# Kernel optimization log

Hardware: AMD Instinct MI355X
Metric: run time of the kernel (lower is better)

Reference implementation:

```python
import jax, jax.numpy as jnp
import numpy as np
from jax import lax

N_STEPS = 8          # fixed-step discretization of t in [0, 1]
GN_GROUPS = 32       # group_norm(width) -> GroupNorm(min(32, width), width)
GN_EPS = 1e-5

# Tsit5 Butcher tableau (c nodes, a stage coeffs, b solution weights; b7 = 0)
_C = (0.161, 0.327, 0.9, 0.9800255409045097, 1.0)
_A = (
    (0.161,),
    (-0.008480655492356989, 0.335480655492357),
    (2.8971530571054935, -6.359448489975075, 4.3622954328695815),
    (5.325864828439257, -11.748883564062828, 7.4955393428898365, -0.09249506636175525),
    (5.86145544294642, -12.92096931784711, 8.159367898576159, -0.071584973281401, -0.028269050394068383),
)
_B = (0.09646076681806523, 0.01, 0.4798896504144996, 1.379008574103742, -3.290069515436081, 2.324710524099774)


def _conv3x3(x, w, b):
    # x: [B, Cin, H, W], w: [Cout, Cin, 3, 3], padding=1, stride=1
    y = lax.conv_general_dilated(x, w, (1, 1), ((1, 1), (1, 1)),
                                 dimension_numbers=("NCHW", "OIHW", "NCHW"))
    return y + b[None, :, None, None]


def _group_norm(x, scale, bias):
    B, C, H, W = x.shape
    xr = x.reshape(B, GN_GROUPS, C // GN_GROUPS, H, W)
    mu = xr.mean(axis=(2, 3, 4), keepdims=True)
    var = xr.var(axis=(2, 3, 4), keepdims=True)
    xn = ((xr - mu) * lax.rsqrt(var + GN_EPS)).reshape(B, C, H, W)
    return xn * scale[None, :, None, None] + bias[None, :, None, None]


def _ode_func(t, x, p):
    # ConcatConv2D: prepend a channel filled with scalar t
    B, _, H, W = x.shape
    tt = jnp.full((B, 1, H, W), t, dtype=x.dtype)
    h = _conv3x3(jnp.concatenate([tt, x], axis=1), p["conv1_w"], p["conv1_b"])
    h = jax.nn.relu(_group_norm(h, p["gn1_scale"], p["gn1_bias"]))
    tt2 = jnp.full((B, 1, H, W), t, dtype=x.dtype)
    h = _conv3x3(jnp.concatenate([tt2, h], axis=1), p["conv2_w"], p["conv2_b"])
    return _group_norm(h, p["gn2_scale"], p["gn2_bias"])


def _tsit5_solve(x, p):
    dt = jnp.float32(1.0 / N_STEPS)

    def step(carry, _):
        y, t = carry
        k1 = _ode_func(t, y, p)
        k2 = _ode_func(t + _C[0] * dt, y + dt * (_A[0][0] * k1), p)
        k3 = _ode_func(t + _C[1] * dt, y + dt * (_A[1][0] * k1 + _A[1][1] * k2), p)
        k4 = _ode_func(t + _C[2] * dt,
                       y + dt * (_A[2][0] * k1 + _A[2][1] * k2 + _A[2][2] * k3), p)
        k5 = _ode_func(t + _C[3] * dt,
                       y + dt * (_A[3][0] * k1 + _A[3][1] * k2 + _A[3][2] * k3 + _A[3][3] * k4), p)
        k6 = _ode_func(t + _C[4] * dt,
                       y + dt * (_A[4][0] * k1 + _A[4][1] * k2 + _A[4][2] * k3
                                 + _A[4][3] * k4 + _A[4][4] * k5), p)
        y_next = y + dt * (_B[0] * k1 + _B[1] * k2 + _B[2] * k3
                           + _B[3] * k4 + _B[4] * k5 + _B[5] * k6)
        return (y_next, t + dt), None

    (yT, _), _ = lax.scan(step, (x, jnp.float32(0.0)), None, length=N_STEPS)
    return yT


def setup_inputs() -> dict:
    key = jax.random.key(0)
    ks = jax.random.split(key, 5)
    B, C, H, W = 64, 64, 32, 32
    cin = C + 1  # concat t channel
    fan_in = cin * 9
    lim = 1.0 / np.sqrt(fan_in)
    x = jax.random.normal(ks[0], (B, C, H, W), dtype=jnp.float32)
    conv1_w = jax.random.uniform(ks[1], (C, cin, 3, 3), jnp.float32, -lim, lim)
    conv1_b = jax.random.uniform(ks[2], (C,), jnp.float32, -lim, lim)
    conv2_w = jax.random.uniform(ks[3], (C, cin, 3, 3), jnp.float32, -lim, lim)
    conv2_b = jax.random.uniform(ks[4], (C,), jnp.float32, -lim, lim)
    return {
        "x": x,
        "conv1_w": conv1_w, "conv1_b": conv1_b,
        "gn1_scale": jnp.ones((C,), jnp.float32), "gn1_bias": jnp.zeros((C,), jnp.float32),
        "conv2_w": conv2_w, "conv2_b": conv2_b,
        "gn2_scale": jnp.ones((C,), jnp.float32), "gn2_bias": jnp.zeros((C,), jnp.float32),
    }


def reference(x, conv1_w, conv1_b, gn1_scale, gn1_bias, conv2_w, conv2_b, gn2_scale, gn2_bias):
    p = {"conv1_w": conv1_w, "conv1_b": conv1_b, "gn1_scale": gn1_scale, "gn1_bias": gn1_bias,
         "conv2_w": conv2_w, "conv2_b": conv2_b, "gn2_scale": gn2_scale, "gn2_bias": gn2_bias}
    return _tsit5_solve(x, p)
```

## Files before the change

kernel.cpp:

```cpp
#include <hip/hip_runtime.h>

typedef __attribute__((ext_vector_type(8))) _Float16 f16x8;
typedef __attribute__((ext_vector_type(4))) float f32x4;
typedef unsigned short u16;

#define BB 64
#define NPIX 1024
#define NELEM (BB*64*NPIX)
#define NRT 8

#define PLANE (6*34*64)

__device__ __forceinline__ int swz8(int c8, int p) {
    return (c8 + ((p + (p >> 2)) & 7)) & 7;
}

__device__ __forceinline__ u16 f2h(float x) {
    _Float16 h = (_Float16)x;
    return __builtin_bit_cast(u16, h);
}
__device__ __forceinline__ float h2f(u16 u) {
    return (float)__builtin_bit_cast(_Float16, u);
}

__global__ __launch_bounds__(256) void prep_w_k(
    const float* __restrict__ w, u16* __restrict__ wt)
{
    int t = blockIdx.x*256 + threadIdx.x;
    if (t >= 4608) return;
    int lane = t & 63;
    int f = t >> 6;
    int g = f & 7;
    int tap = f >> 3;
    int coutblk = g & 3;
    int kc = g >> 2;
    int cout = coutblk*16 + (lane & 15);
    int quad = lane >> 4;
    u16 v[8];
#pragma unroll
    for (int j = 0; j < 8; ++j) {
        int cin = kc*32 + quad*8 + j;
        v[j] = f2h(w[((size_t)cout*65 + (cin+1))*9 + tap]);
    }
    u16* dst = wt + ((size_t)tap*4096 + (g*64 + lane)*8);
    *(ushort4*)(dst)     = make_ushort4(v[0], v[1], v[2], v[3]);
    *(ushort4*)(dst + 4) = make_ushort4(v[4], v[5], v[6], v[7]);
}

__global__ __launch_bounds__(256) void smap_k(
    const float* __restrict__ w, float* __restrict__ smap)
{
    int t = blockIdx.x*256 + threadIdx.x;
    int cout = t >> 10;
    int pix = t & 1023;
    int y = pix >> 5, x = pix & 31;
    float s = 0.f;
#pragma unroll
    for (int dy = 0; dy < 3; ++dy)
#pragma unroll
        for (int dx = 0; dx < 3; ++dx) {
            int yy = y + dy - 1, xx = x + dx - 1;
            if ((unsigned)yy < 32u && (unsigned)xx < 32u)
                s += w[(size_t)cout*65*9 + dy*3 + dx];
        }
    smap[t] = s;
}

template<int MODE, int NK, bool WRITEY>
__global__ __launch_bounds__(512, 4) void conv_mfma_k(
    const float* __restrict__ src0, const u16* __restrict__ srcb,
    const u16* __restrict__ kp0, const u16* __restrict__ kp1,
    const u16* __restrict__ kp2, const u16* __restrict__ kp3,
    const u16* __restrict__ kp4, const u16* __restrict__ kp5,
    float* __restrict__ yout,
    float* __restrict__ part,
    const float* __restrict__ gns, const float* __restrict__ gnb,
    const float* __restrict__ gks, const float* __restrict__ gkb,
    const u16* __restrict__ wt, const float* __restrict__ smap,
    const float* __restrict__ bias, u16* __restrict__ out, float tval,
    int slot_in, int slot_out,
    float a1, float a2, float a3, float a4, float a5, float a6)
{
    __shared__ u16 lds_in[PLANE];
    __shared__ float kaf[6][64];
    __shared__ float kbf[64];
    __shared__ float ps[256], pss[256];
    __shared__ float rg[64], rgq[64];

    const int rt  = blockIdx.x;
    const int b   = blockIdx.y;
    const int tid = threadIdx.x;
    const int wv   = tid >> 6;
    const int lane = tid & 63;
    const int quad = lane >> 4;
    const int n15  = lane & 15;
    const int r0   = wv & 3;
    const int mh   = wv >> 2;

    float4 Y0[2], Y1[2];
    ushort4 H0[2], H1[2];

    auto prim_load = [&](int h) {
#pragma unroll
        for (int uu = 0; uu < 2; ++uu) {
            int ur = tid + uu*512;
            if (ur >= 768) continue;
            int u = h*768 + ur;
            int q4 = u & 7;
            int t2 = u >> 3;
            int rr = t2 % 6;
            int c2 = t2 / 6;
            int gr = rt*4 + rr - 1;
            if ((unsigned)gr < 32u) {
                const size_t base = (((size_t)b*64 + c2*2)*32 + gr)*32 + q4*4;
                if constexpr (MODE == 2) {
                    H0[uu] = *(const ushort4*)(srcb + base);
                    H1[uu] = *(const ushort4*)(srcb + base + 1024);
                } else {
                    Y0[uu] = *(const float4*)(src0 + base);
                    Y1[uu] = *(const float4*)(src0 + base + 1024);
                }
            }
        }
    };

    auto stage_finish = [&](int h) {
#pragma unroll
        for (int uu = 0; uu < 2; ++uu) {
            int ur = tid + uu*512;
            if (ur >= 768) continue;
            int u = h*768 + ur;
            int q4 = u & 7;
            int t2 = u >> 3;
            int rr = t2 % 6;
            int c2 = t2 / 6;
            int gr = rt*4 + rr - 1;
            bool ok = (unsigned)gr < 32u;
            int ch0 = c2*2, ch1 = ch0 + 1;
            float4 a0 = make_float4(0.f,0.f,0.f,0.f), a1v = a0;
            if (ok) {
                const size_t base = (((size_t)b*64 + ch0)*32 + gr)*32 + q4*4;
                if constexpr (MODE == 2) {
                    float A0 = kaf[0][ch0], B0 = kbf[ch0];
                    float A1 = kaf[0][ch1], B1 = kbf[ch1];
                    a0.x = fmaxf(fmaf(h2f(H0[uu].x),A0,B0), 0.f);
                    a0.y = fmaxf(fmaf(h2f(H0[uu].y),A0,B0), 0.f);
                    a0.z = fmaxf(fmaf(h2f(H0[uu].z),A0,B0), 0.f);
                    a0.w = fmaxf(fmaf(h2f(H0[uu].w),A0,B0), 0.f);
                    a1v.x = fmaxf(fmaf(h2f(H1[uu].x),A1,B1), 0.f);
                    a1v.y = fmaxf(fmaf(h2f(H1[uu].y),A1,B1), 0.f);
                    a1v.z = fmaxf(fmaf(h2f(H1[uu].z),A1,B1), 0.f);
                    a1v.w = fmaxf(fmaf(h2f(H1[uu].w),A1,B1), 0.f);
                } else {
                    a0 = Y0[uu]; a1v = Y1[uu];
                    if constexpr (MODE == 1) {
                        float f0 = kbf[ch0], f1 = kbf[ch1];
                        a0.x += f0; a0.y += f0; a0.z += f0; a0.w += f0;
                        a1v.x += f1; a1v.y += f1; a1v.z += f1; a1v.w += f1;
                        const u16* kps[6] = {kp0, kp1, kp2, kp3, kp4, kp5};
#pragma unroll
                        for (int jj = 0; jj < NK; ++jj) {
                            ushort4 kv0 = *(const ushort4*)(kps[jj] + base);
                            ushort4 kv1 = *(const ushort4*)(kps[jj] + base + 1024);
                            float fa0 = kaf[jj][ch0], fa1 = kaf[jj][ch1];
                            a0.x = fmaf(fa0, h2f(kv0.x), a0.x);
                            a0.y = fmaf(fa0, h2f(kv0.y), a0.y);
                            a0.z = fmaf(fa0, h2f(kv0.z), a0.z);
                            a0.w = fmaf(fa0, h2f(kv0.w), a0.w);
                            a1v.x = fmaf(fa1, h2f(kv1.x), a1v.x);
                            a1v.y = fmaf(fa1, h2f(kv1.y), a1v.y);
                            a1v.z = fmaf(fa1, h2f(kv1.z), a1v.z);
                            a1v.w = fmaf(fa1, h2f(kv1.w), a1v.w);
                        }
                    }
                }
                if constexpr (WRITEY) {
                    if (rr >= 1 && rr <= 4) {
                        *(float4*)(yout + base)        = a0;
                        *(float4*)(yout + base + 1024) = a1v;
                    }
                }
            }
            float v0[4] = {a0.x, a0.y, a0.z, a0.w};
            float v1[4] = {a1v.x, a1v.y, a1v.z, a1v.w};
            int c8 = c2 >> 2, cl = c2 & 3;
            int pbase = rr*34 + 1 + q4*4;
#pragma unroll
            for (int j = 0; j < 4; ++j) {
                int p = pbase + j;
                int au = p*64 + swz8(c8, p)*8 + cl*2;
                *(unsigned*)&lds_in[au] =
                    (unsigned)f2h(v0[j]) | ((unsigned)f2h(v1[j]) << 16);
            }
        }
    };

    f32x4 acc[2][2] = {};
    auto mfma_kc = [&](int kc) {
#pragma unroll 3
        for (int tap = 0; tap < 9; ++tap) {
            const int dy = tap / 3;
            const int dx = tap - dy*3;
            const int rowoff = (r0 + dy)*34 + dx;
            const u16* wtap = wt + (size_t)tap*4096;
            f16x8 A[2], Bf[2];
#pragma unroll
            for (int mt = 0; mt < 2; ++mt)
                A[mt] = *(const f16x8*)
                    &wtap[((kc*4 + mh*2 + mt)*64 + lane)*8];
#pragma unroll
            for (int nt = 0; nt < 2; ++nt) {
                int p = rowoff + nt*16 + n15;
                Bf[nt] = *(const f16x8*)&lds_in[p*64 + swz8(kc*4 + quad, p)*8];
            }
#pragma unroll
            for (int mt = 0; mt < 2; ++mt)
#pragma unroll
                for (int nt = 0; nt < 2; ++nt)
                    acc[mt][nt] = __builtin_amdgcn_mfma_f32_16x16x32_f16(
                        A[mt], Bf[nt], acc[mt][nt], 0, 0, 0);
        }
    };

    prim_load(0);

    if constexpr (MODE == 1) {
        if (tid < 64) {
            const float aa[6] = {a1, a2, a3, a4, a5, a6};
            int g = tid >> 1;
            float acb = 0.f;
#pragma unroll
            for (int jj = 0; jj < NK; ++jj) {
                const float4* pp = (const float4*)
                    (part + ((((size_t)(1+jj)*64 + b)*32 + g)*NRT)*2);
                float4 x0 = pp[0], x1 = pp[1], x2 = pp[2], x3 = pp[3];
                float S  = x0.x+x0.z + x1.x+x1.z + x2.x+x2.z + x3.x+x3.z;
                float SS = x0.y+x0.w + x1.y+x1.w + x2.y+x2.w + x3.y+x3.w;
                float mu   = S * (1.f/2048.f);
                float var  = SS * (1.f/2048.f) - mu*mu;
                float rstd = rsqrtf(var + 1e-5f);
                float a = gks[tid]*rstd;
                float c = gkb[tid] - mu*a;
                kaf[jj][tid] = aa[jj]*a;
                acb += aa[jj]*c;
            }
            kbf[tid] = acb;
        }
    } else if constexpr (MODE == 2) {
        if (tid < 64) {
            int g = tid >> 1;
            const float4* pp = (const float4*)
                (part + ((((size_t)slot_in*64 + b)*32 + g)*NRT)*2);
            float4 x0 = pp[0], x1 = pp[1], x2 = pp[2], x3 = pp[3];
            float S  = x0.x+x0.z + x1.x+x1.z + x2.x+x2.z + x3.x+x3.z;
            float SS = x0.y+x0.w + x1.y+x1.w + x2.y+x2.w + x3.y+x3.w;
            float mu   = S * (1.f/2048.f);
            float var  = SS * (1.f/2048.f) - mu*mu;
            float rstd = rsqrtf(var + 1e-5f);
            float a = gns[tid]*rstd;
            kaf[0][tid] = a;
            kbf[tid] = gnb[tid] - mu*a;
        }
    }
    __syncthreads();

    stage_finish(0);
    if (tid < 384) {
        int c2 = tid & 31;
        int t3 = tid >> 5;
        int rr = t3 % 6;
        int e  = t3 / 6;
        int p  = rr*34 + e*33;
        int au = p*64 + swz8(c2 >> 2, p)*8 + (c2 & 3)*2;
        *(unsigned*)&lds_in[au] = 0u;
    }
    __syncthreads();

    prim_load(1);
    mfma_kc(0);
    stage_finish(1);
    __syncthreads();

    mfma_kc(1);

    const int orow = rt*4 + r0;
#pragma unroll
    for (int mt = 0; mt < 2; ++mt) {
#pragma unroll
        for (int r = 0; r < 4; ++r) {
            int cout = mh*32 + mt*16 + quad*4 + r;
            float bs = bias[cout];
            const float* sp = smap + (size_t)cout*1024 + orow*32;
            u16* op = out + (((size_t)b*64 + cout)*32 + orow)*32;
            float v0 = acc[mt][0][r] + bs + tval*sp[n15];
            float v1 = acc[mt][1][r] + bs + tval*sp[16 + n15];
            op[n15]      = f2h(v0);
            op[16 + n15] = f2h(v1);
            float s = v0 + v1;
            float q = v0*v0 + v1*v1;
            s += __shfl_xor(s, 1); q += __shfl_xor(q, 1);
            s += __shfl_xor(s, 2); q += __shfl_xor(q, 2);
            s += __shfl_xor(s, 4); q += __shfl_xor(q, 4);
            s += __shfl_xor(s, 8); q += __shfl_xor(q, 8);
            if (n15 == 0) { ps[r0*64 + cout] = s; pss[r0*64 + cout] = q; }
        }
    }
    __syncthreads();
    if (tid < 64) {
        rg[tid]  = ps[tid]  + ps[64+tid]  + ps[128+tid]  + ps[192+tid];
        rgq[tid] = pss[tid] + pss[64+tid] + pss[128+tid] + pss[192+tid];
    }
    __syncthreads();
    if (tid < 32) {
        float S  = rg[2*tid]  + rg[2*tid+1];
        float SS = rgq[2*tid] + rgq[2*tid+1];
        float* pp = part + ((((size_t)slot_out*64 + b)*32 + tid)*NRT + rt)*2;
        pp[0] = S; pp[1] = SS;
    }
}

__global__ __launch_bounds__(256) void final_combine_k(
    const float* __restrict__ ysrc, float* __restrict__ ydst,
    const u16* __restrict__ k0, const u16* __restrict__ k1,
    const u16* __restrict__ k2, const u16* __restrict__ k3,
    const u16* __restrict__ k4, const u16* __restrict__ k5,
    const float* __restrict__ part,
    const float* __restrict__ g2s, const float* __restrict__ g2b,
    float b0, float b1, float b2, float b3, float b4, float b5)
{
    const int bidx = blockIdx.x;
    const int b = bidx >> 6, ch = bidx & 63, g = ch >> 1;
    const int t = threadIdx.x;
    __shared__ float rs[6][2];
    if (t < 12) {
        int jj = t >> 1, st = t & 1;
        const float* pp = part + ((((size_t)(1+jj)*64 + b)*32 + g)*NRT)*2 + st;
        float v = 0.f;
#pragma unroll
        for (int q = 0; q < NRT; ++q) v += pp[2*q];
        rs[jj][st] = v;
    }
    __syncthreads();
    const float bb[6] = {b0, b1, b2, b3, b4, b5};
    float fa[6], fcs = 0.f;
#pragma unroll
    for (int jj = 0; jj < 6; ++jj) {
        float mu   = rs[jj][0] * (1.f/2048.f);
        float var  = rs[jj][1] * (1.f/2048.f) - mu*mu;
        float rstd = rsqrtf(var + 1e-5f);
        float a = g2s[ch]*rstd;
        float c = g2b[ch] - mu*a;
        fa[jj] = bb[jj]*a;
        fcs   += bb[jj]*c;
    }
    const size_t base = ((size_t)bidx*256 + t)*4;
    float4 r = *(const float4*)(ysrc + base);
    r.x += fcs; r.y += fcs; r.z += fcs; r.w += fcs;
    const u16* kp[6] = {k0, k1, k2, k3, k4, k5};
#pragma unroll
    for (int jj = 0; jj < 6; ++jj) {
        ushort4 kv = *(const ushort4*)(kp[jj] + base);
        r.x = fmaf(fa[jj], h2f(kv.x), r.x);
        r.y = fmaf(fa[jj], h2f(kv.y), r.y);
        r.z = fmaf(fa[jj], h2f(kv.z), r.z);
        r.w = fmaf(fa[jj], h2f(kv.w), r.w);
    }
    *(float4*)(ydst + base) = r;
}


static const double A_[5][5] = {
    {0.161, 0, 0, 0, 0},
    {-0.008480655492356989, 0.335480655492357, 0, 0, 0},
    {2.8971530571054935, -6.359448489975075, 4.3622954328695815, 0, 0},
    {5.325864828439257, -11.748883564062828, 7.4955393428898365, -0.09249506636175525, 0},
    {5.86145544294642, -12.92096931784711, 8.159367898576159, -0.071584973281401, -0.028269050394068383},
};
static const double B_[6] = {
    0.09646076681806523, 0.01, 0.4798896504144996,
    1.379008574103742, -3.290069515436081, 2.324710524099774,
};
static const double C_[5] = {0.161, 0.327, 0.9, 0.9800255409045097, 1.0};

extern "C" void kernel_launch(void* const* d_in, const int* in_sizes, int n_in,
                              void* d_out, int out_size, void* d_ws, size_t ws_size,
                              hipStream_t stream)
{
    const float* x   = (const float*)d_in[0];
    const float* c1w = (const float*)d_in[1];
    const float* c1b = (const float*)d_in[2];
    const float* g1s = (const float*)d_in[3];
    const float* g1b = (const float*)d_in[4];
    const float* c2w = (const float*)d_in[5];
    const float* c2b = (const float*)d_in[6];
    const float* g2s = (const float*)d_in[7];
    const float* g2b = (const float*)d_in[8];

    float* y  = (float*)d_out;
    u16*   wsb = (u16*)d_ws;
    u16*   h  = wsb;
    u16*   k[6];
    for (int i = 0; i < 6; ++i) k[i] = wsb + (size_t)(1 + i) * NELEM;
    u16*   wt1   = wsb + (size_t)7*NELEM;
    u16*   wt2   = wt1 + 73728;
    float* smap1 = (float*)(wt2 + 73728);
    float* smap2 = smap1 + 65536;
    float* part  = smap2 + 65536;
    float* YA    = part + (size_t)7*64*32*8*2;
    float* YB    = YA + NELEM;
    float* yb[2] = {YA, YB};

    const double dt = 0.125;
    const float dtf = 0.125f;

    prep_w_k<<<18, 256, 0, stream>>>(c1w, wt1);
    prep_w_k<<<18, 256, 0, stream>>>(c2w, wt2);
    smap_k<<<256, 256, 0, stream>>>(c1w, smap1);
    smap_k<<<256, 256, 0, stream>>>(c2w, smap2);

    hipMemcpyAsync(YA, x, (size_t)NELEM * sizeof(float),
                   hipMemcpyDeviceToDevice, stream);

    const dim3 cgrid(NRT, BB);
    const float bw0 = (float)(B_[0]*dt), bw1 = (float)(B_[1]*dt),
                bw2 = (float)(B_[2]*dt), bw3 = (float)(B_[3]*dt),
                bw4 = (float)(B_[4]*dt), bw5 = (float)(B_[5]*dt);

    for (int s = 0; s < 8; ++s) {
        const float t0 = dtf * (float)s;
        const float* ys = yb[s & 1];

        if (s == 0) {
            conv_mfma_k<0,0,false><<<cgrid, 512, 0, stream>>>(
                YA, nullptr, nullptr,nullptr,nullptr,nullptr,nullptr,nullptr,
                nullptr, part, g1s, g1b, g2s, g2b,
                wt1, smap1, c1b, h, t0, 0, 0,
                0.f,0.f,0.f,0.f,0.f,0.f);
        } else {
            conv_mfma_k<1,6,true><<<cgrid, 512, 0, stream>>>(
                yb[(s-1)&1], nullptr, k[0],k[1],k[2],k[3],k[4],k[5],
                yb[s&1], part, g1s, g1b, g2s, g2b,
                wt1, smap1, c1b, h, t0, 0, 0,
                bw0, bw1, bw2, bw3, bw4, bw5);
        }
        conv_mfma_k<2,0,false><<<cgrid, 512, 0, stream>>>(
            nullptr, h, nullptr,nullptr,nullptr,nullptr,nullptr,nullptr,
            nullptr, part, g1s, g1b, g2s, g2b,
            wt2, smap2, c2b, k[0], t0, 0, 1,
            0.f,0.f,0.f,0.f,0.f,0.f);

        for (int j = 1; j < 6; ++j) {
            const float tj = t0 + (float)C_[j-1] * dtf;
            float a[5] = {0,0,0,0,0};
            for (int i = 0; i < j; ++i) a[i] = (float)(A_[j-1][i] * dt);
            switch (j) {
            case 1:
                conv_mfma_k<1,1,false><<<cgrid, 512, 0, stream>>>(
                    ys, nullptr, k[0],k[1],k[2],k[3],k[4],k[5],
                    nullptr, part, g1s, g1b, g2s, g2b,
                    wt1, smap1, c1b, h, tj, 0, 0,
                    a[0],a[1],a[2],a[3],a[4],0.f); break;
            case 2:
                conv_mfma_k<1,2,false><<<cgrid, 512, 0, stream>>>(
                    ys, nullptr, k[0],k[1],k[2],k[3],k[4],k[5],
                    nullptr, part, g1s, g1b, g2s, g2b,
                    wt1, smap1, c1b, h, tj, 0, 0,
                    a[0],a[1],a[2],a[3],a[4],0.f); break;
            case 3:
                conv_mfma_k<1,3,false><<<cgrid, 512, 0, stream>>>(
                    ys, nullptr, k[0],k[1],k[2],k[3],k[4],k[5],
                    nullptr, part, g1s, g1b, g2s, g2b,
                    wt1, smap1, c1b, h, tj, 0, 0,
                    a[0],a[1],a[2],a[3],a[4],0.f); break;
            case 4:
                conv_mfma_k<1,4,false><<<cgrid, 512, 0, stream>>>(
                    ys, nullptr, k[0],k[1],k[2],k[3],k[4],k[5],
                    nullptr, part, g1s, g1b, g2s, g2b,
                    wt1, smap1, c1b, h, tj, 0, 0,
                    a[0],a[1],a[2],a[3],a[4],0.f); break;
            default:
                conv_mfma_k<1,5,false><<<cgrid, 512, 0, stream>>>(
                    ys, nullptr, k[0],k[1],k[2],k[3],k[4],k[5],
                    nullptr, part, g1s, g1b, g2s, g2b,
                    wt1, smap1, c1b, h, tj, 0, 0,
                    a[0],a[1],a[2],a[3],a[4],0.f); break;
            }
            conv_mfma_k<2,0,false><<<cgrid, 512, 0, stream>>>(
                nullptr, h, nullptr,nullptr,nullptr,nullptr,nullptr,nullptr,
                nullptr, part, g1s, g1b, g2s, g2b,
                wt2, smap2, c2b, k[j], tj, 0, 1 + j,
                0.f,0.f,0.f,0.f,0.f,0.f);
        }
    }
    final_combine_k<<<4096, 256, 0, stream>>>(
        yb[7 & 1], y, k[0], k[1], k[2], k[3], k[4], k[5], part, g2s, g2b,
        bw0, bw1, bw2, bw3, bw4, bw5);
}
```

Before: 1.835 ms.

## Halve conv tile height to two rows and double row tiles for occupancy

Each conv block now covers two output rows instead of four, so there are twice as many blocks (NRT 16) and the LDS plane shrinks from 6 to 4 input rows. Each wave handles a 16-pixel half-row with two M tiles rather than a full row, and the launch bounds now request 8 blocks per SM. The group-norm partial-sum layout and the reductions that read it are widened to 16 row tiles. The goal is more parallelism and occupancy, at the cost of more halo rereads (4 input rows per 2 output rows instead of 6 per 4) and less weight reuse per block.

```diff
diff --git a/kernel.cpp b/kernel.cpp
--- a/kernel.cpp
+++ b/kernel.cpp
@@ -7,14 +7,13 @@
 #define BB 64
 #define NPIX 1024
 #define NELEM (BB*64*NPIX)
-#define NRT 8
-
-#define PLANE (6*34*64)
+#define NRT 16
+
+#define PLANE (4*34*64)
 
 __device__ __forceinline__ int swz8(int c8, int p) {
     return (c8 + ((p + (p >> 2)) & 7)) & 7;
 }
-
 __device__ __forceinline__ u16 f2h(float x) {
     _Float16 h = (_Float16)x;
     return __builtin_bit_cast(u16, h);
@@ -67,7 +66,7 @@
 }
 
 template<int MODE, int NK, bool WRITEY>
-__global__ __launch_bounds__(512, 4) void conv_mfma_k(
+__global__ __launch_bounds__(512, 8) void conv_mfma_k(
     const float* __restrict__ src0, const u16* __restrict__ srcb,
     const u16* __restrict__ kp0, const u16* __restrict__ kp1,
     const u16* __restrict__ kp2, const u16* __restrict__ kp3,
@@ -94,108 +93,95 @@
     const int lane = tid & 63;
     const int quad = lane >> 4;
     const int n15  = lane & 15;
-    const int r0   = wv & 3;
-    const int mh   = wv >> 2;
-
-    float4 Y0[2], Y1[2];
-    ushort4 H0[2], H1[2];
-
-    auto prim_load = [&](int h) {
-#pragma unroll
-        for (int uu = 0; uu < 2; ++uu) {
-            int ur = tid + uu*512;
-            if (ur >= 768) continue;
-            int u = h*768 + ur;
-            int q4 = u & 7;
-            int t2 = u >> 3;
-            int rr = t2 % 6;
-            int c2 = t2 / 6;
-            int gr = rt*4 + rr - 1;
-            if ((unsigned)gr < 32u) {
-                const size_t base = (((size_t)b*64 + c2*2)*32 + gr)*32 + q4*4;
-                if constexpr (MODE == 2) {
-                    H0[uu] = *(const ushort4*)(srcb + base);
-                    H1[uu] = *(const ushort4*)(srcb + base + 1024);
-                } else {
-                    Y0[uu] = *(const float4*)(src0 + base);
-                    Y1[uu] = *(const float4*)(src0 + base + 1024);
-                }
+    const int r0   = wv & 1;
+    const int mh   = (wv >> 1) & 1;
+    const int nh   = wv >> 2;
+
+    const int q4  = tid & 7;
+    const int t2  = tid >> 3;
+    const int rr  = t2 & 3;
+    const int c2i = t2 >> 2;
+    const int gr  = rt*2 + rr - 1;
+    const bool ok = (unsigned)gr < 32u;
+
+    float4 Y0, Y1;
+    ushort4 H0, H1;
+
+    auto prim_load = [&](int hh) {
+        int c2 = hh*16 + c2i;
+        if (ok) {
+            const size_t base = (((size_t)b*64 + c2*2)*32 + gr)*32 + q4*4;
+            if constexpr (MODE == 2) {
+                H0 = *(const ushort4*)(srcb + base);
+                H1 = *(const ushort4*)(srcb + base + 1024);
+            } else {
+                Y0 = *(const float4*)(src0 + base);
+                Y1 = *(const float4*)(src0 + base + 1024);
             }
         }
     };
 
-    auto stage_finish = [&](int h) {
-#pragma unroll
-        for (int uu = 0; uu < 2; ++uu) {
-            int ur = tid + uu*512;
-            if (ur >= 768) continue;
-            int u = h*768 + ur;
-            int q4 = u & 7;
-            int t2 = u >> 3;
-            int rr = t2 % 6;
-            int c2 = t2 / 6;
-            int gr = rt*4 + rr - 1;
-            bool ok = (unsigned)gr < 32u;
-            int ch0 = c2*2, ch1 = ch0 + 1;
-            float4 a0 = make_float4(0.f,0.f,0.f,0.f), a1v = a0;
-            if (ok) {
-                const size_t base = (((size_t)b*64 + ch0)*32 + gr)*32 + q4*4;
-                if constexpr (MODE == 2) {
-                    float A0 = kaf[0][ch0], B0 = kbf[ch0];
-                    float A1 = kaf[0][ch1], B1 = kbf[ch1];
-                    a0.x = fmaxf(fmaf(h2f(H0[uu].x),A0,B0), 0.f);
-                    a0.y = fmaxf(fmaf(h2f(H0[uu].y),A0,B0), 0.f);
-                    a0.z = fmaxf(fmaf(h2f(H0[uu].z),A0,B0), 0.f);
-                    a0.w = fmaxf(fmaf(h2f(H0[uu].w),A0,B0), 0.f);
-                    a1v.x = fmaxf(fmaf(h2f(H1[uu].x),A1,B1), 0.f);
-                    a1v.y = fmaxf(fmaf(h2f(H1[uu].y),A1,B1), 0.f);
-                    a1v.z = fmaxf(fmaf(h2f(H1[uu].z),A1,B1), 0.f);
-                    a1v.w = fmaxf(fmaf(h2f(H1[uu].w),A1,B1), 0.f);
-                } else {
-                    a0 = Y0[uu]; a1v = Y1[uu];
-                    if constexpr (MODE == 1) {
-                        float f0 = kbf[ch0], f1 = kbf[ch1];
-                        a0.x += f0; a0.y += f0; a0.z += f0; a0.w += f0;
-                        a1v.x += f1; a1v.y += f1; a1v.z += f1; a1v.w += f1;
-                        const u16* kps[6] = {kp0, kp1, kp2, kp3, kp4, kp5};
-#pragma unroll
-                        for (int jj = 0; jj < NK; ++jj) {
-                            ushort4 kv0 = *(const ushort4*)(kps[jj] + base);
-                            ushort4 kv1 = *(const ushort4*)(kps[jj] + base + 1024);
-                            float fa0 = kaf[jj][ch0], fa1 = kaf[jj][ch1];
-                            a0.x = fmaf(fa0, h2f(kv0.x), a0.x);
-                            a0.y = fmaf(fa0, h2f(kv0.y), a0.y);
-                            a0.z = fmaf(fa0, h2f(kv0.z), a0.z);
-                            a0.w = fmaf(fa0, h2f(kv0.w), a0.w);
-                            a1v.x = fmaf(fa1, h2f(kv1.x), a1v.x);
-                            a1v.y = fmaf(fa1, h2f(kv1.y), a1v.y);
-                            a1v.z = fmaf(fa1, h2f(kv1.z), a1v.z);
-                            a1v.w = fmaf(fa1, h2f(kv1.w), a1v.w);
-                        }
+    auto stage_finish = [&](int hh) {
+        int c2 = hh*16 + c2i;
+        int ch0 = c2*2, ch1 = ch0 + 1;
+        float4 a0 = make_float4(0.f,0.f,0.f,0.f), a1v = a0;
+        if (ok) {
+            const size_t base = (((size_t)b*64 + ch0)*32 + gr)*32 + q4*4;
+            if constexpr (MODE == 2) {
+                float A0 = kaf[0][ch0], B0 = kbf[ch0];
+                float A1 = kaf[0][ch1], B1 = kbf[ch1];
+                a0.x = fmaxf(fmaf(h2f(H0.x),A0,B0), 0.f);
+                a0.y = fmaxf(fmaf(h2f(H0.y),A0,B0), 0.f);
+                a0.z = fmaxf(fmaf(h2f(H0.z),A0,B0), 0.f);
+                a0.w = fmaxf(fmaf(h2f(H0.w),A0,B0), 0.f);
+                a1v.x = fmaxf(fmaf(h2f(H1.x),A1,B1), 0.f);
+                a1v.y = fmaxf(fmaf(h2f(H1.y),A1,B1), 0.f);
+                a1v.z = fmaxf(fmaf(h2f(H1.z),A1,B1), 0.f);
+                a1v.w = fmaxf(fmaf(h2f(H1.w),A1,B1), 0.f);
+            } else {
+                a0 = Y0; a1v = Y1;
+                if constexpr (MODE == 1) {
+                    float f0 = kbf[ch0], f1 = kbf[ch1];
+                    a0.x += f0; a0.y += f0; a0.z += f0; a0.w += f0;
+                    a1v.x += f1; a1v.y += f1; a1v.z += f1; a1v.w += f1;
+                    const u16* kps[6] = {kp0, kp1, kp2, kp3, kp4, kp5};
+#pragma unroll
+                    for (int jj = 0; jj < NK; ++jj) {
+                        ushort4 kv0 = *(const ushort4*)(kps[jj] + base);
+                        ushort4 kv1 = *(const ushort4*)(kps[jj] + base + 1024);
+                        float fa0 = kaf[jj][ch0], fa1 = kaf[jj][ch1];
+                        a0.x = fmaf(fa0, h2f(kv0.x), a0.x);
+                        a0.y = fmaf(fa0, h2f(kv0.y), a0.y);
+                        a0.z = fmaf(fa0, h2f(kv0.z), a0.z);
+                        a0.w = fmaf(fa0, h2f(kv0.w), a0.w);
+                        a1v.x = fmaf(fa1, h2f(kv1.x), a1v.x);
+                        a1v.y = fmaf(fa1, h2f(kv1.y), a1v.y);
+                        a1v.z = fmaf(fa1, h2f(kv1.z), a1v.z);
+                        a1v.w = fmaf(fa1, h2f(kv1.w), a1v.w);
                     }
                 }
-                if constexpr (WRITEY) {
-                    if (rr >= 1 && rr <= 4) {
-                        *(float4*)(yout + base)        = a0;
-                        *(float4*)(yout + base + 1024) = a1v;
-                    }
+            }
+            if constexpr (WRITEY) {
+                if (rr >= 1 && rr <= 2) {
+                    *(float4*)(yout + base)        = a0;
+                    *(float4*)(yout + base + 1024) = a1v;
                 }
             }
-            float v0[4] = {a0.x, a0.y, a0.z, a0.w};
-            float v1[4] = {a1v.x, a1v.y, a1v.z, a1v.w};
-            int c8 = c2 >> 2, cl = c2 & 3;
-            int pbase = rr*34 + 1 + q4*4;
-#pragma unroll
-            for (int j = 0; j < 4; ++j) {
-                int p = pbase + j;
-                int au = p*64 + swz8(c8, p)*8 + cl*2;
-                *(unsigned*)&lds_in[au] =
-                    (unsigned)f2h(v0[j]) | ((unsigned)f2h(v1[j]) << 16);
-            }
+        }
+        float v0[4] = {a0.x, a0.y, a0.z, a0.w};
+        float v1[4] = {a1v.x, a1v.y, a1v.z, a1v.w};
+        int c8 = c2 >> 2, cl = c2 & 3;
+        int pbase = rr*34 + 1 + q4*4;
+#pragma unroll
+        for (int j = 0; j < 4; ++j) {
+            int p = pbase + j;
+            int au = p*64 + swz8(c8, p)*8 + cl*2;
+            *(unsigned*)&lds_in[au] =
+                (unsigned)f2h(v0[j]) | ((unsigned)f2h(v1[j]) << 16);
         }
     };
 
-    f32x4 acc[2][2] = {};
+    f32x4 acc[2] = {};
     auto mfma_kc = [&](int kc) {
 #pragma unroll 3
         for (int tap = 0; tap < 9; ++tap) {
@@ -203,22 +189,12 @@
             const int dx = tap - dy*3;
             const int rowoff = (r0 + dy)*34 + dx;
             const u16* wtap = wt + (size_t)tap*4096;
-            f16x8 A[2], Bf[2];
-#pragma unroll
-            for (int mt = 0; mt < 2; ++mt)
-                A[mt] = *(const f16x8*)
-                    &wtap[((kc*4 + mh*2 + mt)*64 + lane)*8];
-#pragma unroll
-            for (int nt = 0; nt < 2; ++nt) {
-                int p = rowoff + nt*16 + n15;
-                Bf[nt] = *(const f16x8*)&lds_in[p*64 + swz8(kc*4 + quad, p)*8];
-            }
-#pragma unroll
-            for (int mt = 0; mt < 2; ++mt)
-#pragma unroll
-                for (int nt = 0; nt < 2; ++nt)
-                    acc[mt][nt] = __builtin_amdgcn_mfma_f32_16x16x32_f16(
-                        A[mt], Bf[nt], acc[mt][nt], 0, 0, 0);
+            f16x8 A0 = *(const f16x8*)&wtap[((kc*4 + mh*2 + 0)*64 + lane)*8];
+            f16x8 A1 = *(const f16x8*)&wtap[((kc*4 + mh*2 + 1)*64 + lane)*8];
+            int p = rowoff + nh*16 + n15;
+            f16x8 Bf = *(const f16x8*)&lds_in[p*64 + swz8(kc*4 + quad, p)*8];
+            acc[0] = __builtin_amdgcn_mfma_f32_16x16x32_f16(A0, Bf, acc[0], 0, 0, 0);
+            acc[1] = __builtin_amdgcn_mfma_f32_16x16x32_f16(A1, Bf, acc[1], 0, 0, 0);
         }
     };
 
@@ -233,9 +209,12 @@
             for (int jj = 0; jj < NK; ++jj) {
                 const float4* pp = (const float4*)
                     (part + ((((size_t)(1+jj)*64 + b)*32 + g)*NRT)*2);
-                float4 x0 = pp[0], x1 = pp[1], x2 = pp[2], x3 = pp[3];
-                float S  = x0.x+x0.z + x1.x+x1.z + x2.x+x2.z + x3.x+x3.z;
-                float SS = x0.y+x0.w + x1.y+x1.w + x2.y+x2.w + x3.y+x3.w;
+                float S = 0.f, SS = 0.f;
+#pragma unroll
+                for (int q = 0; q < 8; ++q) {
+                    float4 v = pp[q];
+                    S += v.x + v.z; SS += v.y + v.w;
+                }
                 float mu   = S * (1.f/2048.f);
                 float var  = SS * (1.f/2048.f) - mu*mu;
                 float rstd = rsqrtf(var + 1e-5f);
@@ -251,9 +230,12 @@
             int g = tid >> 1;
             const float4* pp = (const float4*)
                 (part + ((((size_t)slot_in*64 + b)*32 + g)*NRT)*2);
-            float4 x0 = pp[0], x1 = pp[1], x2 = pp[2], x3 = pp[3];
-            float S  = x0.x+x0.z + x1.x+x1.z + x2.x+x2.z + x3.x+x3.z;
-            float SS = x0.y+x0.w + x1.y+x1.w + x2.y+x2.w + x3.y+x3.w;
+            float S = 0.f, SS = 0.f;
+#pragma unroll
+            for (int q = 0; q < 8; ++q) {
+                float4 v = pp[q];
+                S += v.x + v.z; SS += v.y + v.w;
+            }
             float mu   = S * (1.f/2048.f);
             float var  = SS * (1.f/2048.f) - mu*mu;
             float rstd = rsqrtf(var + 1e-5f);
@@ -265,12 +247,12 @@
     __syncthreads();
 
     stage_finish(0);
-    if (tid < 384) {
+    if (tid < 256) {
         int c2 = tid & 31;
         int t3 = tid >> 5;
-        int rr = t3 % 6;
-        int e  = t3 / 6;
-        int p  = rr*34 + e*33;
+        int hrr = t3 & 3;
+        int e   = t3 >> 2;
+        int p  = hrr*34 + e*33;
         int au = p*64 + swz8(c2 >> 2, p)*8 + (c2 & 3)*2;
         *(unsigned*)&lds_in[au] = 0u;
     }
@@ -283,26 +265,26 @@
 
     mfma_kc(1);
 
-    const int orow = rt*4 + r0;
+    const int orow = rt*2 + r0;
+    const int px   = nh*16 + n15;
 #pragma unroll
     for (int mt = 0; mt < 2; ++mt) {
 #pragma unroll
         for (int r = 0; r < 4; ++r) {
             int cout = mh*32 + mt*16 + quad*4 + r;
-            float bs = bias[cout];
-            const float* sp = smap + (size_t)cout*1024 + orow*32;
-            u16* op = out + (((size_t)b*64 + cout)*32 + orow)*32;
-            float v0 = acc[mt][0][r] + bs + tval*sp[n15];
-            float v1 = acc[mt][1][r] + bs + tval*sp[16 + n15];
-            op[n15]      = f2h(v0);
-            op[16 + n15] = f2h(v1);
-            float s = v0 + v1;
-            float q = v0*v0 + v1*v1;
+            float v = acc[mt][r] + bias[cout]
+                    + tval*smap[(size_t)cout*1024 + orow*32 + px];
+            out[(((size_t)b*64 + cout)*32 + orow)*32 + px] = f2h(v);
+            float s = v;
+            float q = v*v;
             s += __shfl_xor(s, 1); q += __shfl_xor(q, 1);
             s += __shfl_xor(s, 2); q += __shfl_xor(q, 2);
             s += __shfl_xor(s, 4); q += __shfl_xor(q, 4);
             s += __shfl_xor(s, 8); q += __shfl_xor(q, 8);
-            if (n15 == 0) { ps[r0*64 + cout] = s; pss[r0*64 + cout] = q; }
+            if (n15 == 0) {
+                ps[(nh*2 + r0)*64 + cout]  = s;
+                pss[(nh*2 + r0)*64 + cout] = q;
+            }
         }
     }
     __syncthreads();
@@ -406,7 +388,7 @@
     float* smap1 = (float*)(wt2 + 73728);
     float* smap2 = smap1 + 65536;
     float* part  = smap2 + 65536;
-    float* YA    = part + (size_t)7*64*32*8*2;
+    float* YA    = part + (size_t)7*64*32*NRT*2;
     float* YB    = YA + NELEM;
     float* yb[2] = {YA, YB};
 
```

Result: slower. 2.783 ms (+51.7%).
